# Optimization experiments

Measured on AMD Instinct MI355X. Metric: run time of the kernel, lower is better.

Reference implementation:

```python
import jax, jax.numpy as jnp
import numpy as np

B = 2048
IN_DIM = 8192
OUT_DIM = 16384
N_GATES = 16


def setup_inputs() -> dict:
    key = jax.random.key(0)
    k1, k2, k3, k4 = jax.random.split(key, 4)
    x = jax.random.uniform(k1, (B, IN_DIM), dtype=jnp.float32)  # values in [0,1]
    logits = jax.random.normal(k2, (OUT_DIM, N_GATES), dtype=jnp.float32)  # init_std=1.0
    # fixed random connectivity: permutation trick from _pairwise_random_connections
    perm = jax.random.permutation(k3, 2 * OUT_DIM) % IN_DIM
    perm = jax.random.permutation(k4, IN_DIM)[perm]
    c = perm.reshape(2, OUT_DIM)
    return {
        "x": x,
        "logits": logits,
        "a_idx": c[0].astype(jnp.int32),
        "b_idx": c[1].astype(jnp.int32),
    }


def _bin_op_s(a, b, p):
    # a, b: (B, out_dim); p: (out_dim, 16) gate probabilities, broadcast over batch.
    # Weighted sum of the 16 real-valued relaxations of 2-input Boolean gates
    # (standard DiffLogic gate ordering; gate 0 is constant 0, gate 15 constant 1).
    ab = a * b
    return (
        p[:, 1] * ab                          # AND
        + p[:, 2] * (a - ab)                  # a AND NOT b
        + p[:, 3] * a                         # a
        + p[:, 4] * (b - ab)                  # NOT a AND b
        + p[:, 5] * b                         # b
        + p[:, 6] * (a + b - 2.0 * ab)        # XOR
        + p[:, 7] * (a + b - ab)              # OR
        + p[:, 8] * (1.0 - (a + b - ab))      # NOR
        + p[:, 9] * (1.0 - (a + b - 2.0 * ab))  # XNOR
        + p[:, 10] * (1.0 - b)                # NOT b
        + p[:, 11] * (1.0 - b + ab)           # a OR NOT b
        + p[:, 12] * (1.0 - a)                # NOT a
        + p[:, 13] * (1.0 - a + ab)           # NOT a OR b
        + p[:, 14] * (1.0 - ab)               # NAND
        + p[:, 15]                            # constant 1
    )


def reference(x, logits, a_idx, b_idx):
    # Gather the two inputs of each output gate: (B, out_dim)
    a = x[:, a_idx]
    b = x[:, b_idx]
    # Training mode: softmax relaxation over the 16 gates per node.
    p = jax.nn.softmax(logits, axis=-1)
    return _bin_op_s(a, b, p)
```

## Files before the change

### kernel.cpp

```cpp
#include <hip/hip_runtime.h>
#include <hip/hip_bf16.h>

#define IN_DIM  8192
#define OUT_DIM 16384
#define BATCH   2048
#define NG      16
#define RROWS   4
#define TPB     512
#define NITER   (OUT_DIM / 4 / TPB)

typedef float        f32x4 __attribute__((ext_vector_type(4)));
typedef unsigned int u32x2 __attribute__((ext_vector_type(2)));
typedef unsigned int u32x4 __attribute__((ext_vector_type(4)));


__device__ __forceinline__ void collapse_weights(const float* __restrict__ l,
                                                 float& w_ab, float& w_a,
                                                 float& w_b, float& w_c) {
    float v[NG];
    float m = -1e30f;
#pragma unroll
    for (int k = 0; k < NG; ++k) { v[k] = l[k]; m = fmaxf(m, v[k]); }
    float s = 0.f;
#pragma unroll
    for (int k = 0; k < NG; ++k) { v[k] = __expf(v[k] - m); s += v[k]; }
    float inv = 1.0f / s;
#pragma unroll
    for (int k = 0; k < NG; ++k) v[k] *= inv;
    w_ab = v[1] - v[2] - v[4] - 2.f * v[6] - v[7] + v[8] + 2.f * v[9]
         + v[11] + v[13] - v[14];
    w_a  = v[2] + v[3] + v[6] + v[7] - v[8] - v[9] - v[12] - v[13];
    w_b  = v[4] + v[5] + v[6] + v[7] - v[8] - v[9] - v[10] - v[11];
    w_c  = v[8] + v[9] + v[10] + v[11] + v[12] + v[13] + v[14] + v[15];
}

__global__ __launch_bounds__(256) void gate_weights_kernel(
    const float* __restrict__ logits,
    const int* __restrict__ a_idx, const int* __restrict__ b_idx,
    float* __restrict__ ws) {
    int j = blockIdx.x * blockDim.x + threadIdx.x;
    if (j >= OUT_DIM) return;
    float w_ab, w_a, w_b, w_c;
    collapse_weights(logits + (size_t)j * NG, w_ab, w_a, w_b, w_c);
    ws[j]               = w_ab;
    ws[j +     OUT_DIM] = w_a;
    ws[j + 2 * OUT_DIM] = w_b;
    ws[j + 3 * OUT_DIM] = w_c;
    unsigned int* pk = (unsigned int*)(ws + 4 * OUT_DIM);
    pk[j] = (unsigned int)a_idx[j] | ((unsigned int)b_idx[j] << 16);
}

__device__ __forceinline__ float bf16_hi_to_f(unsigned int u) {
    union { unsigned int i; float f; } c; c.i = u & 0xFFFF0000u; return c.f;
}
__device__ __forceinline__ float bf16_lo_to_f(unsigned int u) {
    union { unsigned int i; float f; } c; c.i = u << 16; return c.f;
}

__global__ __launch_bounds__(TPB, 4) void gate_eval_kernel(
    const float* __restrict__ x,
    const float* __restrict__ ws,
    f32x4* __restrict__ out4) {
    __shared__ u32x2 rowsp[IN_DIM];
    const int i0 = blockIdx.x * RROWS;

    const f32x4* wab4 = (const f32x4*)(ws);
    const f32x4* wa4  = (const f32x4*)(ws + OUT_DIM);
    const f32x4* wb4  = (const f32x4*)(ws + 2 * OUT_DIM);
    const f32x4* wc4  = (const f32x4*)(ws + 3 * OUT_DIM);
    const u32x4* pk4  = (const u32x4*)(ws + 4 * OUT_DIM);

    u32x4 pkb[2];
    f32x4 wabb[2], wab_[2], wbb[2], wcb[2];
    {
        int j4 = threadIdx.x;
        pkb[0]  = pk4[j4];
        wabb[0] = wab4[j4];
        wab_[0] = wa4[j4];
        wbb[0]  = wb4[j4];
        wcb[0]  = wc4[j4];
    }

    const float* x0 = x + (size_t)i0 * IN_DIM;
#pragma unroll
    for (int t = 0; t < IN_DIM / TPB; ++t) {
        int k = threadIdx.x + t * TPB;
        unsigned short b0 = __bfloat16_as_ushort(__float2bfloat16(x0[k]));
        unsigned short b1 = __bfloat16_as_ushort(__float2bfloat16(x0[k + IN_DIM]));
        unsigned short b2 = __bfloat16_as_ushort(__float2bfloat16(x0[k + 2 * IN_DIM]));
        unsigned short b3 = __bfloat16_as_ushort(__float2bfloat16(x0[k + 3 * IN_DIM]));
        u32x2 p;
        p.x = (unsigned int)b0 | ((unsigned int)b1 << 16);
        p.y = (unsigned int)b2 | ((unsigned int)b3 << 16);
        rowsp[k] = p;
    }
    __syncthreads();

    f32x4* o0 = out4 + (size_t)i0 * (OUT_DIM / 4);
    f32x4* o1 = o0 + (OUT_DIM / 4);
    f32x4* o2 = o1 + (OUT_DIM / 4);
    f32x4* o3 = o2 + (OUT_DIM / 4);

#pragma unroll
    for (int k = 0; k < NITER; ++k) {
        const int cur = k & 1, nxt = cur ^ 1;
        if (k + 1 < NITER) {
            int j4n = threadIdx.x + (k + 1) * TPB;
            pkb[nxt]  = pk4[j4n];
            wabb[nxt] = wab4[j4n];
            wab_[nxt] = wa4[j4n];
            wbb[nxt]  = wb4[j4n];
            wcb[nxt]  = wc4[j4n];
        }
        int j4 = threadIdx.x + k * TPB;
        u32x4 pk = pkb[cur];
        f32x4 wab = wabb[cur], wa = wab_[cur], wb = wbb[cur], wc = wcb[cur];
        f32x4 r0, r1, r2, r3;
#pragma unroll
        for (int c = 0; c < 4; ++c) {
            u32x2 va = rowsp[pk[c] & 0xFFFFu];
            u32x2 vb = rowsp[pk[c] >> 16];
            float a0 = bf16_lo_to_f(va.x), a1 = bf16_hi_to_f(va.x);
            float a2 = bf16_lo_to_f(va.y), a3 = bf16_hi_to_f(va.y);
            float b0 = bf16_lo_to_f(vb.x), b1 = bf16_hi_to_f(vb.x);
            float b2 = bf16_lo_to_f(vb.y), b3 = bf16_hi_to_f(vb.y);
            r0[c] = fmaf(wab[c], a0 * b0, fmaf(wa[c], a0, fmaf(wb[c], b0, wc[c])));
            r1[c] = fmaf(wab[c], a1 * b1, fmaf(wa[c], a1, fmaf(wb[c], b1, wc[c])));
            r2[c] = fmaf(wab[c], a2 * b2, fmaf(wa[c], a2, fmaf(wb[c], b2, wc[c])));
            r3[c] = fmaf(wab[c], a3 * b3, fmaf(wa[c], a3, fmaf(wb[c], b3, wc[c])));
        }
        __builtin_nontemporal_store(r0, &o0[j4]);
        __builtin_nontemporal_store(r1, &o1[j4]);
        __builtin_nontemporal_store(r2, &o2[j4]);
        __builtin_nontemporal_store(r3, &o3[j4]);
    }
}

__global__ __launch_bounds__(256) void gate_eval_fused_kernel(
    const float* __restrict__ x,
    const float* __restrict__ logits,
    const int* __restrict__ a_idx,
    const int* __restrict__ b_idx,
    float* __restrict__ out) {
    __shared__ float row[IN_DIM];
    const int i = blockIdx.x;
    const f32x4* xr = (const f32x4*)(x + (size_t)i * IN_DIM);
    f32x4* rv = (f32x4*)row;
#pragma unroll
    for (int t = 0; t < IN_DIM / 4 / 256; ++t)
        rv[threadIdx.x + t * 256] = xr[threadIdx.x + t * 256];
    __syncthreads();
    float* o = out + (size_t)i * OUT_DIM;
    for (int k = 0; k < OUT_DIM / 256; ++k) {
        int j = threadIdx.x + k * 256;
        float w_ab, w_a, w_b, w_c;
        collapse_weights(logits + (size_t)j * NG, w_ab, w_a, w_b, w_c);
        float a = row[a_idx[j]], b = row[b_idx[j]];
        o[j] = fmaf(w_ab, a * b, fmaf(w_a, a, fmaf(w_b, b, w_c)));
    }
}

extern "C" void kernel_launch(void* const* d_in, const int* in_sizes, int n_in,
                              void* d_out, int out_size, void* d_ws, size_t ws_size,
                              hipStream_t stream) {
    const float* x      = (const float*)d_in[0];
    const float* logits = (const float*)d_in[1];
    const int*   a_idx  = (const int*)d_in[2];
    const int*   b_idx  = (const int*)d_in[3];
    float* out = (float*)d_out;

    const size_t ws_need = (size_t)(4 * OUT_DIM) * sizeof(float)
                         + (size_t)OUT_DIM * sizeof(unsigned int);
    if (ws_size >= ws_need && d_ws != nullptr) {
        float* ws = (float*)d_ws;
        gate_weights_kernel<<<OUT_DIM / 256, 256, 0, stream>>>(
            logits, a_idx, b_idx, ws);
        gate_eval_kernel<<<BATCH / RROWS, TPB, 0, stream>>>(
            x, ws, (f32x4*)out);
    } else {
        gate_eval_fused_kernel<<<BATCH, 256, 0, stream>>>(
            x, logits, a_idx, b_idx, out);
    }
}
```

Baseline: 40.37 us.

## Fuse weight precompute into eval kernel via cooperative grid sync

Merges the gate-weight softmax/collapse kernel into the evaluation kernel using a cooperative launch. Each block computes a slice of the collapsed weights and packed indices while staging its x rows into shared memory, then a grid-wide barrier precedes the main loop. This removes a separate kernel launch and its serialization gap, at the cost of a grid sync, cooperative launch overhead, and the requirement that all 512 blocks be co-resident. The old two-kernel path remains as a fallback, and the shared-memory fallback for a missing workspace is removed.

```diff
diff --git a/kernel.cpp b/kernel.cpp
--- a/kernel.cpp
+++ b/kernel.cpp
@@ -1,5 +1,8 @@
 #include <hip/hip_runtime.h>
 #include <hip/hip_bf16.h>
+#include <hip/hip_cooperative_groups.h>
+
+namespace cg = cooperative_groups;
 
 #define IN_DIM  8192
 #define OUT_DIM 16384
@@ -7,6 +10,8 @@
 #define NG      16
 #define RROWS   4
 #define TPB     512
+#define NBLK    (BATCH / RROWS)
+#define CPB     (OUT_DIM / NBLK)
 #define NITER   (OUT_DIM / 4 / TPB)
 
 typedef float        f32x4 __attribute__((ext_vector_type(4)));
@@ -34,22 +39,6 @@
     w_c  = v[8] + v[9] + v[10] + v[11] + v[12] + v[13] + v[14] + v[15];
 }
 
-__global__ __launch_bounds__(256) void gate_weights_kernel(
-    const float* __restrict__ logits,
-    const int* __restrict__ a_idx, const int* __restrict__ b_idx,
-    float* __restrict__ ws) {
-    int j = blockIdx.x * blockDim.x + threadIdx.x;
-    if (j >= OUT_DIM) return;
-    float w_ab, w_a, w_b, w_c;
-    collapse_weights(logits + (size_t)j * NG, w_ab, w_a, w_b, w_c);
-    ws[j]               = w_ab;
-    ws[j +     OUT_DIM] = w_a;
-    ws[j + 2 * OUT_DIM] = w_b;
-    ws[j + 3 * OUT_DIM] = w_c;
-    unsigned int* pk = (unsigned int*)(ws + 4 * OUT_DIM);
-    pk[j] = (unsigned int)a_idx[j] | ((unsigned int)b_idx[j] << 16);
-}
-
 __device__ __forceinline__ float bf16_hi_to_f(unsigned int u) {
     union { unsigned int i; float f; } c; c.i = u & 0xFFFF0000u; return c.f;
 }
@@ -57,13 +46,9 @@
     union { unsigned int i; float f; } c; c.i = u << 16; return c.f;
 }
 
-__global__ __launch_bounds__(TPB, 4) void gate_eval_kernel(
-    const float* __restrict__ x,
-    const float* __restrict__ ws,
-    f32x4* __restrict__ out4) {
-    __shared__ u32x2 rowsp[IN_DIM];
-    const int i0 = blockIdx.x * RROWS;
-
+__device__ __forceinline__ void eval_main_loop(
+    const float* __restrict__ ws, const u32x2* rowsp,
+    f32x4* __restrict__ out4, int i0) {
     const f32x4* wab4 = (const f32x4*)(ws);
     const f32x4* wa4  = (const f32x4*)(ws + OUT_DIM);
     const f32x4* wb4  = (const f32x4*)(ws + 2 * OUT_DIM);
@@ -80,21 +65,6 @@
         wbb[0]  = wb4[j4];
         wcb[0]  = wc4[j4];
     }
-
-    const float* x0 = x + (size_t)i0 * IN_DIM;
-#pragma unroll
-    for (int t = 0; t < IN_DIM / TPB; ++t) {
-        int k = threadIdx.x + t * TPB;
-        unsigned short b0 = __bfloat16_as_ushort(__float2bfloat16(x0[k]));
-        unsigned short b1 = __bfloat16_as_ushort(__float2bfloat16(x0[k + IN_DIM]));
-        unsigned short b2 = __bfloat16_as_ushort(__float2bfloat16(x0[k + 2 * IN_DIM]));
-        unsigned short b3 = __bfloat16_as_ushort(__float2bfloat16(x0[k + 3 * IN_DIM]));
-        u32x2 p;
-        p.x = (unsigned int)b0 | ((unsigned int)b1 << 16);
-        p.y = (unsigned int)b2 | ((unsigned int)b3 << 16);
-        rowsp[k] = p;
-    }
-    __syncthreads();
 
     f32x4* o0 = out4 + (size_t)i0 * (OUT_DIM / 4);
     f32x4* o1 = o0 + (OUT_DIM / 4);
@@ -136,28 +106,84 @@
     }
 }
 
-__global__ __launch_bounds__(256) void gate_eval_fused_kernel(
+__global__ __launch_bounds__(TPB, 4) void fused_gate_kernel(
     const float* __restrict__ x,
     const float* __restrict__ logits,
     const int* __restrict__ a_idx,
     const int* __restrict__ b_idx,
-    float* __restrict__ out) {
-    __shared__ float row[IN_DIM];
-    const int i = blockIdx.x;
-    const f32x4* xr = (const f32x4*)(x + (size_t)i * IN_DIM);
-    f32x4* rv = (f32x4*)row;
-#pragma unroll
-    for (int t = 0; t < IN_DIM / 4 / 256; ++t)
-        rv[threadIdx.x + t * 256] = xr[threadIdx.x + t * 256];
-    __syncthreads();
-    float* o = out + (size_t)i * OUT_DIM;
-    for (int k = 0; k < OUT_DIM / 256; ++k) {
-        int j = threadIdx.x + k * 256;
+    float* __restrict__ ws,
+    f32x4* __restrict__ out4) {
+    __shared__ u32x2 rowsp[IN_DIM];
+    const int i0 = blockIdx.x * RROWS;
+
+    const float* x0 = x + (size_t)i0 * IN_DIM;
+#pragma unroll
+    for (int t = 0; t < IN_DIM / TPB; ++t) {
+        int k = threadIdx.x + t * TPB;
+        unsigned short b0 = __bfloat16_as_ushort(__float2bfloat16(x0[k]));
+        unsigned short b1 = __bfloat16_as_ushort(__float2bfloat16(x0[k + IN_DIM]));
+        unsigned short b2 = __bfloat16_as_ushort(__float2bfloat16(x0[k + 2 * IN_DIM]));
+        unsigned short b3 = __bfloat16_as_ushort(__float2bfloat16(x0[k + 3 * IN_DIM]));
+        u32x2 p;
+        p.x = (unsigned int)b0 | ((unsigned int)b1 << 16);
+        p.y = (unsigned int)b2 | ((unsigned int)b3 << 16);
+        rowsp[k] = p;
+    }
+
+    if (threadIdx.x < CPB) {
+        int j = blockIdx.x * CPB + threadIdx.x;
         float w_ab, w_a, w_b, w_c;
         collapse_weights(logits + (size_t)j * NG, w_ab, w_a, w_b, w_c);
-        float a = row[a_idx[j]], b = row[b_idx[j]];
-        o[j] = fmaf(w_ab, a * b, fmaf(w_a, a, fmaf(w_b, b, w_c)));
-    }
+        ws[j]               = w_ab;
+        ws[j +     OUT_DIM] = w_a;
+        ws[j + 2 * OUT_DIM] = w_b;
+        ws[j + 3 * OUT_DIM] = w_c;
+        unsigned int* pk = (unsigned int*)(ws + 4 * OUT_DIM);
+        pk[j] = (unsigned int)a_idx[j] | ((unsigned int)b_idx[j] << 16);
+    }
+
+    cg::this_grid().sync();
+    eval_main_loop(ws, rowsp, out4, i0);
+}
+
+
+__global__ __launch_bounds__(256) void gate_weights_kernel(
+    const float* __restrict__ logits,
+    const int* __restrict__ a_idx, const int* __restrict__ b_idx,
+    float* __restrict__ ws) {
+    int j = blockIdx.x * blockDim.x + threadIdx.x;
+    if (j >= OUT_DIM) return;
+    float w_ab, w_a, w_b, w_c;
+    collapse_weights(logits + (size_t)j * NG, w_ab, w_a, w_b, w_c);
+    ws[j]               = w_ab;
+    ws[j +     OUT_DIM] = w_a;
+    ws[j + 2 * OUT_DIM] = w_b;
+    ws[j + 3 * OUT_DIM] = w_c;
+    unsigned int* pk = (unsigned int*)(ws + 4 * OUT_DIM);
+    pk[j] = (unsigned int)a_idx[j] | ((unsigned int)b_idx[j] << 16);
+}
+
+__global__ __launch_bounds__(TPB, 4) void gate_eval_kernel(
+    const float* __restrict__ x,
+    const float* __restrict__ ws,
+    f32x4* __restrict__ out4) {
+    __shared__ u32x2 rowsp[IN_DIM];
+    const int i0 = blockIdx.x * RROWS;
+    const float* x0 = x + (size_t)i0 * IN_DIM;
+#pragma unroll
+    for (int t = 0; t < IN_DIM / TPB; ++t) {
+        int k = threadIdx.x + t * TPB;
+        unsigned short b0 = __bfloat16_as_ushort(__float2bfloat16(x0[k]));
+        unsigned short b1 = __bfloat16_as_ushort(__float2bfloat16(x0[k + IN_DIM]));
+        unsigned short b2 = __bfloat16_as_ushort(__float2bfloat16(x0[k + 2 * IN_DIM]));
+        unsigned short b3 = __bfloat16_as_ushort(__float2bfloat16(x0[k + 3 * IN_DIM]));
+        u32x2 p;
+        p.x = (unsigned int)b0 | ((unsigned int)b1 << 16);
+        p.y = (unsigned int)b2 | ((unsigned int)b3 << 16);
+        rowsp[k] = p;
+    }
+    __syncthreads();
+    eval_main_loop(ws, rowsp, out4, i0);
 }
 
 extern "C" void kernel_launch(void* const* d_in, const int* in_sizes, int n_in,
@@ -167,18 +193,16 @@
     const float* logits = (const float*)d_in[1];
     const int*   a_idx  = (const int*)d_in[2];
     const int*   b_idx  = (const int*)d_in[3];
-    float* out = (float*)d_out;
-
-    const size_t ws_need = (size_t)(4 * OUT_DIM) * sizeof(float)
-                         + (size_t)OUT_DIM * sizeof(unsigned int);
-    if (ws_size >= ws_need && d_ws != nullptr) {
-        float* ws = (float*)d_ws;
+    float* ws  = (float*)d_ws;
+    f32x4* o4  = (f32x4*)d_out;
+
+    void* args[6] = {(void*)&x, (void*)&logits, (void*)&a_idx,
+                     (void*)&b_idx, (void*)&ws, (void*)&o4};
+    hipError_t e = hipLaunchCooperativeKernel(
+        (const void*)fused_gate_kernel, dim3(NBLK), dim3(TPB), args, 0, stream);
+    if (e != hipSuccess) {
         gate_weights_kernel<<<OUT_DIM / 256, 256, 0, stream>>>(
             logits, a_idx, b_idx, ws);
-        gate_eval_kernel<<<BATCH / RROWS, TPB, 0, stream>>>(
-            x, ws, (f32x4*)out);
-    } else {
-        gate_eval_fused_kernel<<<BATCH, 256, 0, stream>>>(
-            x, logits, a_idx, b_idx, out);
-    }
-}
+        gate_eval_kernel<<<NBLK, TPB, 0, stream>>>(x, ws, o4);
+    }
+}
```

Result: slower. 99.35 us (+146.1%).
